# Performance work log

Measured on AMD Instinct MI355X. Metric: run time of the kernel, lower is better.

## Reference

```python
import jax, jax.numpy as jnp
import numpy as np

H = 2048   # hidden_size
SW = 256   # stack_width
SD = 200   # stack_depth
V = 128    # input_size (vocab)
O = 128    # output_size


def setup_inputs() -> dict:
    key = jax.random.key(0)
    ks = jax.random.split(key, 14)
    s = 0.02
    return {
        'inp': jax.random.randint(ks[0], (1,), 0, V),
        'hidden': jax.random.normal(ks[1], (1, 1, H), jnp.float32),
        'stack': jax.random.normal(ks[2], (1, SD, SW), jnp.float32),
        'emb': jax.random.normal(ks[3], (V, H), jnp.float32) * s,
        'Wc': jax.random.normal(ks[4], (3, H), jnp.float32) * s,
        'bc': jax.random.normal(ks[5], (3,), jnp.float32) * s,
        'Ws': jax.random.normal(ks[6], (SW, H), jnp.float32) * s,
        'bs': jax.random.normal(ks[7], (SW,), jnp.float32) * s,
        'W_ih': jax.random.normal(ks[8], (3 * H, H + SW), jnp.float32) * s,
        'b_ih': jax.random.normal(ks[9], (3 * H,), jnp.float32) * s,
        'W_hh': jax.random.normal(ks[10], (3 * H, H), jnp.float32) * s,
        'b_hh': jax.random.normal(ks[11], (3 * H,), jnp.float32) * s,
        'Wd': jax.random.normal(ks[12], (O, H), jnp.float32) * s,
        'bd': jax.random.normal(ks[13], (O,), jnp.float32) * s,
    }


def reference(inp, hidden, stack, emb, Wc, bc, Ws, bs, W_ih, b_ih, W_hh, b_hh, Wd, bd):
    # embedding: inp.view(1,-1) -> (1,1) -> (1,1,H)
    x = emb[inp.reshape(1, -1)]
    # stack controls: softmax(Linear(hidden.squeeze(0)))  -> (1,3)
    ctrl = jax.nn.softmax(hidden[0] @ Wc.T + bc, axis=1)
    # stack input: tanh(Linear(hidden)) -> (1,1,SW); permute(1,0,2) is identity for (1,1,SW)
    s_in = jnp.tanh(hidden @ Ws.T + bs)
    s_in = jnp.transpose(s_in, (1, 0, 2))  # (batch=1, 1, SW)
    # differentiable stack push/pop/no-op
    B, _, W = stack.shape
    a_push = ctrl[:, 0][:, None, None]
    a_pop = ctrl[:, 1][:, None, None]
    a_noop = ctrl[:, 2][:, None, None]
    zeros_bot = jnp.zeros((B, 1, W), dtype=stack.dtype)
    stack_down = jnp.concatenate([stack[:, 1:], zeros_bot], axis=1)
    stack_up = jnp.concatenate([s_in, stack[:, :-1]], axis=1)
    new_stack = a_noop * stack + a_push * stack_up + a_pop * stack_down
    stack_top = new_stack[:, 0, :][None]  # (1,1,SW)
    # single-step GRU (PyTorch gate order: r, z, n)
    gin = jnp.concatenate([x, stack_top], axis=2).reshape(1, -1)  # (1, H+SW)
    h = hidden.reshape(1, -1)                                      # (1, H)
    gi = gin @ W_ih.T + b_ih
    gh = h @ W_hh.T + b_hh
    r = jax.nn.sigmoid(gi[:, :H] + gh[:, :H])
    z = jax.nn.sigmoid(gi[:, H:2 * H] + gh[:, H:2 * H])
    n = jnp.tanh(gi[:, 2 * H:] + r * gh[:, 2 * H:])
    h_new = (1.0 - z) * n + z * h
    out = h_new @ Wd.T + bd  # (1, O)
    return out, h_new[None], new_stack
```

## Files before the change

kernel.cpp:

```cpp
#include <hip/hip_runtime.h>
#include <math.h>

#define H   2048
#define SW  256
#define SD  200
#define GIN (H + SW)
#define G3H (3 * H)
#define OO  128

#define STOP_OFF 8
#define GI_OFF   512
#define GH_OFF   (GI_OFF + G3H)

__device__ __forceinline__ float wave_reduce(float v) {
#pragma unroll
    for (int off = 32; off > 0; off >>= 1)
        v += __shfl_down(v, off, 64);
    return v;
}

__device__ __forceinline__ float sigmoidf(float x) {
    return 1.f / (1.f + expf(-x));
}

__device__ __forceinline__ float dot4(float4 a, float4 b) {
    return a.x * b.x + a.y * b.y + a.z * b.z + a.w * b.w;
}

__global__ __launch_bounds__(256) void k_stack(
        const float* __restrict__ hidden,
        const float* __restrict__ stack,
        const float* __restrict__ Wc,
        const float* __restrict__ bc,
        const float* __restrict__ Ws,
        const float* __restrict__ bs,
        float* __restrict__ ws,
        float* __restrict__ out_stack ) {
    __shared__ float sc[3];
    int tid = threadIdx.x;
    if (tid < 64) {
        float c0 = 0.f, c1 = 0.f, c2 = 0.f;
        for (int k = tid; k < H; k += 64) {
            float hv = hidden[k];
            c0 += hv * Wc[k];
            c1 += hv * Wc[H + k];
            c2 += hv * Wc[2 * H + k];
        }
        c0 = wave_reduce(c0); c1 = wave_reduce(c1); c2 = wave_reduce(c2);
        if (tid == 0) {
            c0 += bc[0]; c1 += bc[1]; c2 += bc[2];
            float m = fmaxf(c0, fmaxf(c1, c2));
            float e0 = expf(c0 - m), e1 = expf(c1 - m), e2 = expf(c2 - m);
            float inv = 1.f / (e0 + e1 + e2);
            sc[0] = e0 * inv;
            sc[1] = e1 * inv;
            sc[2] = e2 * inv;
        }
    }
    __syncthreads();
    float a_push = sc[0], a_pop = sc[1], a_noop = sc[2];
    int b = blockIdx.x;
    if (b < 64) {
        int wave = tid >> 6, lane = tid & 63;
        int row = b * 4 + wave;
        const float4* h4 = (const float4*)hidden;
        const float4* w4 = (const float4*)(Ws + row * H);
        float sum = 0.f;
#pragma unroll
        for (int i = 0; i < 8; ++i) {
            float4 a = h4[lane + i * 64];
            float4 c = w4[lane + i * 64];
            sum += dot4(a, c);
        }
        sum = wave_reduce(sum);
        if (lane == 0) {
            float s = tanhf(sum + bs[row]);
            float top = a_noop * stack[row] + a_push * s + a_pop * stack[SW + row];
            ws[STOP_OFF + row] = top;
            out_stack[row] = top;
        }
    } else {
        int rbase = 1 + (b - 64) * 4;
#pragma unroll
        for (int r = 0; r < 4; ++r) {
            int row = rbase + r;
            if (row >= SD) break;
            int idx = row * SW + tid;
            float dn = (row < SD - 1) ? stack[idx + SW] : 0.f;
            out_stack[idx] = a_noop * stack[idx] + a_push * stack[idx - SW] + a_pop * dn;
        }
    }
}

__global__ __launch_bounds__(256) void k_gemv(
        const float* __restrict__ hidden,
        const float* __restrict__ emb,
        const int* __restrict__ inp,
        const float* __restrict__ W_ih, const float* __restrict__ b_ih,
        const float* __restrict__ W_hh, const float* __restrict__ b_hh,
        float* __restrict__ ws) {
    __shared__ __align__(16) float vec[GIN];
    int b = blockIdx.x;
    int tid = threadIdx.x;
    bool is_gi = (b < 384);
    if (is_gi) {
        int e = inp[0];
        const float* er = emb + (long)e * H;
        for (int k = tid; k < H; k += 256) vec[k] = er[k];
        for (int k = H + tid; k < GIN; k += 256) vec[k] = ws[STOP_OFF + (k - H)];
    } else {
        for (int k = tid; k < H; k += 256) vec[k] = hidden[k];
    }
    __syncthreads();
    int wave = tid >> 6, lane = tid & 63;
    int rbase = (is_gi ? b : b - 384) * 16 + wave * 4;
    const float* W    = is_gi ? W_ih : W_hh;
    const float* bias = is_gi ? b_ih : b_hh;
    int K  = is_gi ? GIN : H;
    int K4 = K >> 2;
    const float4* v4 = (const float4*)vec;
    const float4* w0 = (const float4*)(W + (long)(rbase + 0) * K);
    const float4* w1 = (const float4*)(W + (long)(rbase + 1) * K);
    const float4* w2 = (const float4*)(W + (long)(rbase + 2) * K);
    const float4* w3 = (const float4*)(W + (long)(rbase + 3) * K);
    float s0 = 0.f, s1 = 0.f, s2 = 0.f, s3 = 0.f;
    int i = lane;
    for (; i + 64 < K4; i += 128) {
        int j = i + 64;
        float4 a0  = v4[i],  a1  = v4[j];
        float4 b00 = w0[i],  b01 = w0[j];
        float4 b10 = w1[i],  b11 = w1[j];
        float4 b20 = w2[i],  b21 = w2[j];
        float4 b30 = w3[i],  b31 = w3[j];
        s0 += dot4(a0, b00) + dot4(a1, b01);
        s1 += dot4(a0, b10) + dot4(a1, b11);
        s2 += dot4(a0, b20) + dot4(a1, b21);
        s3 += dot4(a0, b30) + dot4(a1, b31);
    }
    if (i < K4) {
        float4 a0 = v4[i];
        s0 += dot4(a0, w0[i]);
        s1 += dot4(a0, w1[i]);
        s2 += dot4(a0, w2[i]);
        s3 += dot4(a0, w3[i]);
    }
    s0 = wave_reduce(s0);
    s1 = wave_reduce(s1);
    s2 = wave_reduce(s2);
    s3 = wave_reduce(s3);
    float* dst = ws + (is_gi ? GI_OFF : GH_OFF);
    if (lane == 0) {
        dst[rbase + 0] = s0 + bias[rbase + 0];
        dst[rbase + 1] = s1 + bias[rbase + 1];
        dst[rbase + 2] = s2 + bias[rbase + 2];
        dst[rbase + 3] = s3 + bias[rbase + 3];
    }
}

__global__ __launch_bounds__(256) void k_out(
        const float* __restrict__ hidden,
        const float* __restrict__ Wd, const float* __restrict__ bd,
        const float* __restrict__ ws,
        float* __restrict__ d_out) {
    __shared__ __align__(16) float hn[H];
    int tid = threadIdx.x;
    const float* gi = ws + GI_OFF;
    const float* gh = ws + GH_OFF;
    for (int i = tid; i < H; i += 256) {
        float r = sigmoidf(gi[i] + gh[i]);
        float z = sigmoidf(gi[H + i] + gh[H + i]);
        float n = tanhf(gi[2 * H + i] + r * gh[2 * H + i]);
        float v = (1.f - z) * n + z * hidden[i];
        hn[i] = v;
        if (blockIdx.x == 0) d_out[OO + i] = v;
    }
    __syncthreads();
    int wave = tid >> 6, lane = tid & 63;
    int row = blockIdx.x * 4 + wave;
    const float4* h4 = (const float4*)hn;
    const float4* w4 = (const float4*)(Wd + (long)row * H);
    float sum = 0.f;
#pragma unroll
    for (int i = 0; i < 8; ++i) {
        float4 a = h4[lane + i * 64];
        float4 c = w4[lane + i * 64];
        sum += dot4(a, c);
    }
    sum = wave_reduce(sum);
    if (lane == 0) d_out[row] = sum + bd[row];
}

extern "C" void kernel_launch(void* const* d_in, const int* in_sizes, int n_in,
                              void* d_out, int out_size, void* d_ws, size_t ws_size,
                              hipStream_t stream) {
    const int*   inp    = (const int*)d_in[0];
    const float* hidden = (const float*)d_in[1];
    const float* stack  = (const float*)d_in[2];
    const float* emb    = (const float*)d_in[3];
    const float* Wc     = (const float*)d_in[4];
    const float* bc     = (const float*)d_in[5];
    const float* Ws     = (const float*)d_in[6];
    const float* bs     = (const float*)d_in[7];
    const float* W_ih   = (const float*)d_in[8];
    const float* b_ih   = (const float*)d_in[9];
    const float* W_hh   = (const float*)d_in[10];
    const float* b_hh   = (const float*)d_in[11];
    const float* Wd     = (const float*)d_in[12];
    const float* bd     = (const float*)d_in[13];
    float* out = (float*)d_out;
    float* ws  = (float*)d_ws;

    k_stack<<<114, 256, 0, stream>>>(hidden, stack, Wc, bc, Ws, bs, ws, out + OO + H);
    k_gemv<<<768, 256, 0, stream>>>(hidden, emb, inp, W_ih, b_ih, W_hh, b_hh, ws);
    k_out<<<32, 256, 0, stream>>>(hidden, Wd, bd, ws, out);
}
```

Before: 180.4 us.

## Split W_ih GEMV to break stack dependency and fuse into two launches

The input-gate GEMV is split into its embedding part, which has no dependency on the stack-top vector, and a small stack-top part. The embedding part is fused with the hidden GEMV and the stack update into one launch. The stack-top slice of W_ih is computed in the final kernel, and an atomic-counter spin barrier makes the 32 output blocks wait for all 384 partial blocks before the GRU nonlinearity and output projection. This removes one kernel launch and the serialization of the big GEMV behind the stack kernel, at the cost of a grid-wide spin wait that depends on all blocks being co-resident or scheduled in order.

```diff
diff --git a/kernel.cpp b/kernel.cpp
--- a/kernel.cpp
+++ b/kernel.cpp
@@ -11,6 +11,7 @@
 #define STOP_OFF 8
 #define GI_OFF   512
 #define GH_OFF   (GI_OFF + G3H)
+#define GIS_OFF  (GH_OFF + G3H)
 
 __device__ __forceinline__ float wave_reduce(float v) {
 #pragma unroll
@@ -27,17 +28,73 @@
     return a.x * b.x + a.y * b.y + a.z * b.z + a.w * b.w;
 }
 
-__global__ __launch_bounds__(256) void k_stack(
+__global__ __launch_bounds__(256) void k_main(
         const float* __restrict__ hidden,
         const float* __restrict__ stack,
         const float* __restrict__ Wc,
         const float* __restrict__ bc,
         const float* __restrict__ Ws,
         const float* __restrict__ bs,
+        const float* __restrict__ emb,
+        const int* __restrict__ inp,
+        const float* __restrict__ W_ih, const float* __restrict__ b_ih,
+        const float* __restrict__ W_hh, const float* __restrict__ b_hh,
         float* __restrict__ ws,
         float* __restrict__ out_stack ) {
+    int b = blockIdx.x;
+    int tid = threadIdx.x;
+
+    if (b < 768) {
+        __shared__ __align__(16) float vec[H];
+        bool is_gh = (b < 384);
+        if (is_gh) {
+            for (int k = tid; k < H; k += 256) vec[k] = hidden[k];
+        } else {
+            const float* er = emb + (long)inp[0] * H;
+            for (int k = tid; k < H; k += 256) vec[k] = er[k];
+        }
+        __syncthreads();
+        int wave = tid >> 6, lane = tid & 63;
+        int rbase = (is_gh ? b : b - 384) * 16 + wave * 4;
+        const float* W    = is_gh ? W_hh : W_ih;
+        const float* bias = is_gh ? b_hh : b_ih;
+        long stride = is_gh ? H : GIN;
+        const float4* v4 = (const float4*)vec;
+        const float4* w0 = (const float4*)(W + (rbase + 0) * stride);
+        const float4* w1 = (const float4*)(W + (rbase + 1) * stride);
+        const float4* w2 = (const float4*)(W + (rbase + 2) * stride);
+        const float4* w3 = (const float4*)(W + (rbase + 3) * stride);
+        float s0 = 0.f, s1 = 0.f, s2 = 0.f, s3 = 0.f;
+#pragma unroll
+        for (int ii = 0; ii < 4; ++ii) {
+            int i = lane + ii * 128;
+            int j = i + 64;
+            float4 a0  = v4[i],  a1  = v4[j];
+            float4 b00 = w0[i],  b01 = w0[j];
+            float4 b10 = w1[i],  b11 = w1[j];
+            float4 b20 = w2[i],  b21 = w2[j];
+            float4 b30 = w3[i],  b31 = w3[j];
+            s0 += dot4(a0, b00) + dot4(a1, b01);
+            s1 += dot4(a0, b10) + dot4(a1, b11);
+            s2 += dot4(a0, b20) + dot4(a1, b21);
+            s3 += dot4(a0, b30) + dot4(a1, b31);
+        }
+        s0 = wave_reduce(s0);
+        s1 = wave_reduce(s1);
+        s2 = wave_reduce(s2);
+        s3 = wave_reduce(s3);
+        float* dst = ws + (is_gh ? GH_OFF : GI_OFF);
+        if (lane == 0) {
+            dst[rbase + 0] = s0 + bias[rbase + 0];
+            dst[rbase + 1] = s1 + bias[rbase + 1];
+            dst[rbase + 2] = s2 + bias[rbase + 2];
+            dst[rbase + 3] = s3 + bias[rbase + 3];
+        }
+        return;
+    }
+
     __shared__ float sc[3];
-    int tid = threadIdx.x;
+    if (b == 768 && tid == 0) ((unsigned*)ws)[0] = 0u;
     if (tid < 64) {
         float c0 = 0.f, c1 = 0.f, c2 = 0.f;
         for (int k = tid; k < H; k += 64) {
@@ -59,19 +116,15 @@
     }
     __syncthreads();
     float a_push = sc[0], a_pop = sc[1], a_noop = sc[2];
-    int b = blockIdx.x;
-    if (b < 64) {
+    if (b < 832) {
         int wave = tid >> 6, lane = tid & 63;
-        int row = b * 4 + wave;
+        int row = (b - 768) * 4 + wave;
         const float4* h4 = (const float4*)hidden;
         const float4* w4 = (const float4*)(Ws + row * H);
         float sum = 0.f;
 #pragma unroll
-        for (int i = 0; i < 8; ++i) {
-            float4 a = h4[lane + i * 64];
-            float4 c = w4[lane + i * 64];
-            sum += dot4(a, c);
-        }
+        for (int i = 0; i < 8; ++i)
+            sum += dot4(h4[lane + i * 64], w4[lane + i * 64]);
         sum = wave_reduce(sum);
         if (lane == 0) {
             float s = tanhf(sum + bs[row]);
@@ -80,7 +133,7 @@
             out_stack[row] = top;
         }
     } else {
-        int rbase = 1 + (b - 64) * 4;
+        int rbase = 1 + (b - 832) * 4;
 #pragma unroll
         for (int r = 0; r < 4; ++r) {
             int row = rbase + r;
@@ -92,100 +145,74 @@
     }
 }
 
-__global__ __launch_bounds__(256) void k_gemv(
+__global__ __launch_bounds__(256) void k_fin(
         const float* __restrict__ hidden,
-        const float* __restrict__ emb,
-        const int* __restrict__ inp,
-        const float* __restrict__ W_ih, const float* __restrict__ b_ih,
-        const float* __restrict__ W_hh, const float* __restrict__ b_hh,
-        float* __restrict__ ws) {
-    __shared__ __align__(16) float vec[GIN];
+        const float* __restrict__ W_ih,
+        const float* __restrict__ Wd, const float* __restrict__ bd,
+        float* __restrict__ ws,
+        float* __restrict__ d_out) {
+    __shared__ __align__(16) float st[SW];
+    __shared__ __align__(16) float hn[H];
     int b = blockIdx.x;
     int tid = threadIdx.x;
-    bool is_gi = (b < 384);
-    if (is_gi) {
-        int e = inp[0];
-        const float* er = emb + (long)e * H;
-        for (int k = tid; k < H; k += 256) vec[k] = er[k];
-        for (int k = H + tid; k < GIN; k += 256) vec[k] = ws[STOP_OFF + (k - H)];
-    } else {
-        for (int k = tid; k < H; k += 256) vec[k] = hidden[k];
-    }
+    if (tid < SW) st[tid] = ws[STOP_OFF + tid];
     __syncthreads();
     int wave = tid >> 6, lane = tid & 63;
-    int rbase = (is_gi ? b : b - 384) * 16 + wave * 4;
-    const float* W    = is_gi ? W_ih : W_hh;
-    const float* bias = is_gi ? b_ih : b_hh;
-    int K  = is_gi ? GIN : H;
-    int K4 = K >> 2;
-    const float4* v4 = (const float4*)vec;
-    const float4* w0 = (const float4*)(W + (long)(rbase + 0) * K);
-    const float4* w1 = (const float4*)(W + (long)(rbase + 1) * K);
-    const float4* w2 = (const float4*)(W + (long)(rbase + 2) * K);
-    const float4* w3 = (const float4*)(W + (long)(rbase + 3) * K);
-    float s0 = 0.f, s1 = 0.f, s2 = 0.f, s3 = 0.f;
-    int i = lane;
-    for (; i + 64 < K4; i += 128) {
-        int j = i + 64;
-        float4 a0  = v4[i],  a1  = v4[j];
-        float4 b00 = w0[i],  b01 = w0[j];
-        float4 b10 = w1[i],  b11 = w1[j];
-        float4 b20 = w2[i],  b21 = w2[j];
-        float4 b30 = w3[i],  b31 = w3[j];
-        s0 += dot4(a0, b00) + dot4(a1, b01);
-        s1 += dot4(a0, b10) + dot4(a1, b11);
-        s2 += dot4(a0, b20) + dot4(a1, b21);
-        s3 += dot4(a0, b30) + dot4(a1, b31);
-    }
-    if (i < K4) {
-        float4 a0 = v4[i];
-        s0 += dot4(a0, w0[i]);
-        s1 += dot4(a0, w1[i]);
-        s2 += dot4(a0, w2[i]);
-        s3 += dot4(a0, w3[i]);
-    }
+    int rbase = b * 16 + wave * 4;
+    const float4* v4 = (const float4*)st;
+    float4 a = v4[lane];
+    const float4* w0 = (const float4*)(W_ih + (long)(rbase + 0) * GIN + H);
+    const float4* w1 = (const float4*)(W_ih + (long)(rbase + 1) * GIN + H);
+    const float4* w2 = (const float4*)(W_ih + (long)(rbase + 2) * GIN + H);
+    const float4* w3 = (const float4*)(W_ih + (long)(rbase + 3) * GIN + H);
+    float s0 = dot4(a, w0[lane]);
+    float s1 = dot4(a, w1[lane]);
+    float s2 = dot4(a, w2[lane]);
+    float s3 = dot4(a, w3[lane]);
     s0 = wave_reduce(s0);
     s1 = wave_reduce(s1);
     s2 = wave_reduce(s2);
     s3 = wave_reduce(s3);
-    float* dst = ws + (is_gi ? GI_OFF : GH_OFF);
     if (lane == 0) {
-        dst[rbase + 0] = s0 + bias[rbase + 0];
-        dst[rbase + 1] = s1 + bias[rbase + 1];
-        dst[rbase + 2] = s2 + bias[rbase + 2];
-        dst[rbase + 3] = s3 + bias[rbase + 3];
-    }
-}
-
-__global__ __launch_bounds__(256) void k_out(
-        const float* __restrict__ hidden,
-        const float* __restrict__ Wd, const float* __restrict__ bd,
-        const float* __restrict__ ws,
-        float* __restrict__ d_out) {
-    __shared__ __align__(16) float hn[H];
-    int tid = threadIdx.x;
-    const float* gi = ws + GI_OFF;
-    const float* gh = ws + GH_OFF;
+        float* gis = ws + GIS_OFF;
+        gis[rbase + 0] = s0;
+        gis[rbase + 1] = s1;
+        gis[rbase + 2] = s2;
+        gis[rbase + 3] = s3;
+    }
+    __syncthreads();
+    if (tid == 0) {
+        __threadfence();
+        atomicAdd((unsigned*)ws, 1u);
+    }
+    if (b >= 32) return;
+
+    if (tid == 0) {
+        while (atomicAdd((unsigned*)ws, 0u) < 384u)
+            __builtin_amdgcn_s_sleep(2);
+        __threadfence();
+    }
+    __syncthreads();
+
+    const float* gi  = ws + GI_OFF;
+    const float* gh  = ws + GH_OFF;
+    const float* gis = ws + GIS_OFF;
     for (int i = tid; i < H; i += 256) {
-        float r = sigmoidf(gi[i] + gh[i]);
-        float z = sigmoidf(gi[H + i] + gh[H + i]);
-        float n = tanhf(gi[2 * H + i] + r * gh[2 * H + i]);
+        float r = sigmoidf(gi[i] + gis[i] + gh[i]);
+        float z = sigmoidf(gi[H + i] + gis[H + i] + gh[H + i]);
+        float n = tanhf(gi[2 * H + i] + gis[2 * H + i] + r * gh[2 * H + i]);
         float v = (1.f - z) * n + z * hidden[i];
         hn[i] = v;
-        if (blockIdx.x == 0) d_out[OO + i] = v;
-    }
-    __syncthreads();
-    int wave = tid >> 6, lane = tid & 63;
-    int row = blockIdx.x * 4 + wave;
-    const float4* h4 = (const float4*)hn;
-    const float4* w4 = (const float4*)(Wd + (long)row * H);
+        if (b == 0) d_out[OO + i] = v;
+    }
+    __syncthreads();
+    int row = b * 4 + wave;
+    const float4* h4  = (const float4*)hn;
+    const float4* wd4 = (const float4*)(Wd + (long)row * H);
     float sum = 0.f;
 #pragma unroll
-    for (int i = 0; i < 8; ++i) {
-        float4 a = h4[lane + i * 64];
-        float4 c = w4[lane + i * 64];
-        sum += dot4(a, c);
-    }
+    for (int i = 0; i < 8; ++i)
+        sum += dot4(h4[lane + i * 64], wd4[lane + i * 64]);
     sum = wave_reduce(sum);
     if (lane == 0) d_out[row] = sum + bd[row];
 }
@@ -210,7 +237,7 @@
     float* out = (float*)d_out;
     float* ws  = (float*)d_ws;
 
-    k_stack<<<114, 256, 0, stream>>>(hidden, stack, Wc, bc, Ws, bs, ws, out + OO + H);
-    k_gemv<<<768, 256, 0, stream>>>(hidden, emb, inp, W_ih, b_ih, W_hh, b_hh, ws);
-    k_out<<<32, 256, 0, stream>>>(hidden, Wd, bd, ws, out);
-}
+    k_main<<<882, 256, 0, stream>>>(hidden, stack, Wc, bc, Ws, bs, emb, inp,
+                                    W_ih, b_ih, W_hh, b_hh, ws, out + OO + H);
+    k_fin<<<384, 256, 0, stream>>>(hidden, W_ih, Wd, bd, ws, out);
+}
```

Result: no change. 180.2 us (-0.1%).
